# Performance work log

Measured on AMD Instinct MI355X. Metric: run time of the kernel, lower is better.

Reference implementation:

```python
import jax, jax.numpy as jnp
import numpy as np

B, L, DK, DV, H = 2, 2048, 512, 512, 8
DH_K = DK // H  # 64
DH_V = DV // H  # 64


def setup_inputs() -> dict:
    key = jax.random.key(0)
    ks = jax.random.split(key, 6)
    scale_w = 1.0 / np.sqrt(DK)
    return {
        "keys": jax.random.normal(ks[0], (B, L, DK), dtype=jnp.float32),
        "queries": jax.random.normal(ks[1], (B, L, DK), dtype=jnp.float32),
        "values": jax.random.normal(ks[2], (B, L, DV), dtype=jnp.float32),
        "WQ": jax.random.normal(ks[3], (H, DK, DH_K), dtype=jnp.float32) * scale_w,
        "WK": jax.random.normal(ks[4], (H, DK, DH_K), dtype=jnp.float32) * scale_w,
        "WV": jax.random.normal(ks[5], (H, DV, DH_V), dtype=jnp.float32) * scale_w,
    }


def reference(keys, queries, values, WQ, WK, WV):
    # Per-head projections, vectorized over all H heads at once.
    Q = jnp.einsum('bld,hde->bhle', queries, WQ)   # [B,H,Lq,dh]
    K = jnp.einsum('bld,hde->bhle', keys, WK)      # [B,H,Lk,dh]
    V = jnp.einsum('bld,hde->bhle', values, WV)    # [B,H,Lk,dv_h]
    Lk = keys.shape[1]
    # NOTE: original scales by sqrt(seq_len_k), not sqrt(head_dim).
    y = jnp.einsum('bhqe,bhke->bhqk', Q, K) / jnp.sqrt(jnp.float32(Lk))
    # NOTE: original applies softmax over torch dim=1 of [B,Lq,Lk],
    # i.e. the QUERY axis (axis=2 here in [B,H,Lq,Lk]).
    z = jax.nn.softmax(y, axis=2)
    out = jnp.einsum('bhqk,bhke->bhqe', z, V)      # [B,H,Lq,dv_h]
    # Concat heads on the feature dim (same order as torch.concat(..., 2)).
    Bq, Hh, Lq, Dh = out.shape
    return out.transpose(0, 2, 1, 3).reshape(Bq, Lq, Hh * Dh)
```

## Files before the change

### kernel.cpp

```cpp
#include <hip/hip_runtime.h>
#include <hip/hip_bf16.h>

#define LL 2048
#define DM 512
#define SCALE 0.02209708691207961f

typedef unsigned short u16;
typedef __attribute__((ext_vector_type(8))) short short8;
typedef __attribute__((ext_vector_type(4))) short short4v;
typedef __attribute__((ext_vector_type(4))) float f32x4;

#define XAQ_OFF 0u
#define XAK_OFF 2097152u
#define XAV_OFF 4194304u
#define WB_OFF  6291456u
#define QA_OFF  7077888u
#define KA_OFF  9175040u
#define VB_OFF  11272192u

__device__ __forceinline__ u16 f2bf(float f) {
  union { float f; unsigned u; } v; v.f = f;
  unsigned r = v.u + 0x7fff + ((v.u >> 16) & 1);
  return (u16)(r >> 16);
}
__device__ __forceinline__ float bf2f(u16 u) {
  union { unsigned u; float f; } v; v.u = ((unsigned)u) << 16; return v.f;
}
__device__ __forceinline__ size_t frag_idx(int bh, int t64, int w, int c, int lane) {
  return ((((size_t)(bh * 32 + t64) * 4 + w) * 2 + c) * 64 + lane) * 8;
}
__device__ __forceinline__ size_t vb_idx(int bh, int kt, int w, int et, int lane) {
  return ((((size_t)(bh * 32 + kt) * 4 + w) * 4 + et) * 64 + lane) * 4;
}

__global__ __launch_bounds__(256) void prep_kernel(
    const float* __restrict__ queries, const float* __restrict__ keys,
    const float* __restrict__ values, const float* __restrict__ WQ,
    const float* __restrict__ WK, const float* __restrict__ WV,
    u16* __restrict__ wsb) {
  int t = threadIdx.x;
  int blk = blockIdx.x;
  if (blk < 768) {
    int tens = blk >> 8;
    int grp  = blk & 255;
    const float* src = (tens == 0 ? queries : tens == 1 ? keys : values) +
                       (size_t)grp * 16 * 512;
    __shared__ __align__(16) u16 Xs[16][520];
#pragma unroll
    for (int rep = 0; rep < 8; ++rep) {
      int f4 = t + rep * 256;
      int row = f4 >> 7, c4 = f4 & 127;
      float4 v = *(const float4*)(src + (size_t)row * 512 + c4 * 4);
      short4v o;
      o[0] = (short)f2bf(v.x); o[1] = (short)f2bf(v.y);
      o[2] = (short)f2bf(v.z); o[3] = (short)f2bf(v.w);
      *(short4v*)&Xs[row][c4 * 4] = o;
    }
    __syncthreads();
    u16* dst = wsb + (tens == 0 ? XAQ_OFF : tens == 1 ? XAK_OFF : XAV_OFF) +
               (size_t)grp * 16 * 64 * 8;
#pragma unroll
    for (int rep = 0; rep < 4; ++rep) {
      int o = t + rep * 256;
      int kt = o >> 6, lane = o & 63;
      int quad = lane >> 4, l16 = lane & 15;
      short8 v = *(const short8*)&Xs[l16][kt * 32 + quad * 8];
      *(short8*)(dst + (size_t)o * 8) = v;
    }
  } else {
    int c2 = (blk - 768) * 256 + t;
    int lane = c2 & 63;
    int nt = (c2 >> 6) & 3;
    int kt = (c2 >> 8) & 15;
    int h  = (c2 >> 12) & 7;
    int z  = c2 >> 15;
    int quad = lane >> 4, l16 = lane & 15;
    const float* W = (z == 0) ? WQ : (z == 1) ? WK : WV;
    const float* src = W + ((size_t)h * DM + kt * 32 + quad * 8) * 64 + nt * 16 + l16;
    short8 o;
#pragma unroll
    for (int j = 0; j < 8; ++j) o[j] = (short)f2bf(src[(size_t)j * 64]);
    *(short8*)(wsb + WB_OFF + (size_t)c2 * 8) = o;
  }
}

__global__ __launch_bounds__(256) void proj_kernel(u16* __restrict__ wsb) {
  int t = threadIdx.x;
  int lane = t & 63, w = t >> 6, quad = lane >> 4, l16 = lane & 15;
  int z = blockIdx.z, bh = blockIdx.y, b = bh >> 3, h = bh & 7;
  int QT = blockIdx.x;

  const u16* Bw = wsb + WB_OFF + ((size_t)(z * 8 + h) * 16) * 4 * 64 * 8;
  const u16* Ab = wsb + (z == 0 ? XAQ_OFF : z == 1 ? XAK_OFF : XAV_OFF) +
      (((size_t)b * 128 + QT * 4 + w) * 16) * 64 * 8;

  f32x4 acc[4];
#pragma unroll
  for (int nt = 0; nt < 4; ++nt) acc[nt] = (f32x4){0.f, 0.f, 0.f, 0.f};

#pragma unroll 4
  for (int kt = 0; kt < 16; ++kt) {
    short8 a = *(const short8*)(Ab + ((size_t)kt * 64 + lane) * 8);
#pragma unroll
    for (int nt = 0; nt < 4; ++nt) {
      short8 bb = *(const short8*)(Bw + (((size_t)kt * 4 + nt) * 64 + lane) * 8);
      acc[nt] = __builtin_amdgcn_mfma_f32_16x16x32_bf16(a, bb, acc[nt], 0, 0, 0);
    }
  }

  __shared__ float Cs[64][68];
  float sc = (z == 0) ? SCALE : 1.0f;
#pragma unroll
  for (int nt = 0; nt < 4; ++nt)
#pragma unroll
    for (int r = 0; r < 4; ++r)
      Cs[w * 16 + quad * 4 + r][nt * 16 + l16] = acc[nt][r] * sc;
  __syncthreads();

  if (z < 2) {
    u16* base = wsb + (z == 0 ? QA_OFF : KA_OFF);
#pragma unroll
    for (int c = 0; c < 2; ++c) {
      const float* srcr = &Cs[w * 16 + l16][c * 32 + quad * 8];
      short8 o;
#pragma unroll
      for (int j = 0; j < 8; ++j) o[j] = (short)f2bf(srcr[j]);
      *(short8*)(base + frag_idx(bh, QT, w, c, lane)) = o;
    }
  } else {
#pragma unroll
    for (int et = 0; et < 4; ++et) {
      short4v o;
#pragma unroll
      for (int j = 0; j < 4; ++j)
        o[j] = (short)f2bf(Cs[w * 16 + quad * 4 + j][et * 16 + l16]);
      *(short4v*)(wsb + VB_OFF + vb_idx(bh, QT, w, et, lane)) = o;
    }
  }
}

__global__ __launch_bounds__(256) void stats_kernel(u16* __restrict__ wsb) {
  int t = threadIdx.x;
  int lane = t & 63, w = t >> 6, quad = lane >> 4, l16 = lane & 15;
  int bh = blockIdx.y;
  int KT = blockIdx.x;

  short8 ka[4][2];
#pragma unroll
  for (int mt = 0; mt < 4; ++mt)
#pragma unroll
    for (int c = 0; c < 2; ++c)
      ka[mt][c] = *(const short8*)(wsb + KA_OFF + frag_idx(bh, KT, mt, c, lane));

  float rs[4][4];
#pragma unroll
  for (int mt = 0; mt < 4; ++mt)
#pragma unroll
    for (int r = 0; r < 4; ++r) rs[mt][r] = 0.f;

  for (int qt = 0; qt < 32; ++qt) {
    short8 qb0 = *(const short8*)(wsb + QA_OFF + frag_idx(bh, qt, w, 0, lane));
    short8 qb1 = *(const short8*)(wsb + QA_OFF + frag_idx(bh, qt, w, 1, lane));
#pragma unroll
    for (int mt = 0; mt < 4; ++mt) {
      f32x4 y = (f32x4){0.f, 0.f, 0.f, 0.f};
      y = __builtin_amdgcn_mfma_f32_16x16x32_bf16(ka[mt][0], qb0, y, 0, 0, 0);
      y = __builtin_amdgcn_mfma_f32_16x16x32_bf16(ka[mt][1], qb1, y, 0, 0, 0);
#pragma unroll
      for (int r = 0; r < 4; ++r) rs[mt][r] += __expf(y[r]);
    }
  }
#pragma unroll
  for (int mt = 0; mt < 4; ++mt)
#pragma unroll
    for (int r = 0; r < 4; ++r) {
      rs[mt][r] += __shfl_xor(rs[mt][r], 1);
      rs[mt][r] += __shfl_xor(rs[mt][r], 2);
      rs[mt][r] += __shfl_xor(rs[mt][r], 4);
      rs[mt][r] += __shfl_xor(rs[mt][r], 8);
    }

  __shared__ float Sred[4][64];
  __shared__ float Ss[64];
  if (l16 == 0) {
#pragma unroll
    for (int mt = 0; mt < 4; ++mt)
#pragma unroll
      for (int r = 0; r < 4; ++r)
        Sred[w][mt * 16 + quad * 4 + r] = rs[mt][r];
  }
  __syncthreads();
  if (t < 64) Ss[t] = 1.0f / (Sred[0][t] + Sred[1][t] + Sred[2][t] + Sred[3][t]);
  __syncthreads();

#pragma unroll
  for (int et = 0; et < 4; ++et) {
    u16* p = wsb + VB_OFF + vb_idx(bh, KT, w, et, lane);
    short4v v = *(short4v*)p;
#pragma unroll
    for (int j = 0; j < 4; ++j)
      v[j] = (short)f2bf(bf2f((u16)v[j]) * Ss[w * 16 + quad * 4 + j]);
    *(short4v*)p = v;
  }
}

__global__ __launch_bounds__(256, 2) void attn_kernel(const u16* __restrict__ wsb,
                                                      float* __restrict__ out) {
  int t = threadIdx.x;
  int lane = t & 63, w = t >> 6, quad = lane >> 4, l16 = lane & 15;
  int bh = blockIdx.y, b = bh >> 3, h = bh & 7;
  int QT = blockIdx.x, qbase = QT * 64;

  short8 qf[4][2];
#pragma unroll
  for (int nt = 0; nt < 4; ++nt)
#pragma unroll
    for (int c = 0; c < 2; ++c)
      qf[nt][c] = *(const short8*)(wsb + QA_OFF + frag_idx(bh, QT, nt, c, lane));

  f32x4 oacc[4][4];
#pragma unroll
  for (int nt = 0; nt < 4; ++nt)
#pragma unroll
    for (int et = 0; et < 4; ++et) oacc[nt][et] = (f32x4){0.f, 0.f, 0.f, 0.f};

  for (int kt = 0; kt < 32; ++kt) {
    short8 ka0 = *(const short8*)(wsb + KA_OFF + frag_idx(bh, kt, w, 0, lane));
    short8 ka1 = *(const short8*)(wsb + KA_OFF + frag_idx(bh, kt, w, 1, lane));
    short4v vb[4];
#pragma unroll
    for (int et = 0; et < 4; ++et)
      vb[et] = *(const short4v*)(wsb + VB_OFF + vb_idx(bh, kt, w, et, lane));

#pragma unroll
    for (int nt = 0; nt < 4; ++nt) {
      f32x4 y = (f32x4){0.f, 0.f, 0.f, 0.f};
      y = __builtin_amdgcn_mfma_f32_16x16x32_bf16(ka0, qf[nt][0], y, 0, 0, 0);
      y = __builtin_amdgcn_mfma_f32_16x16x32_bf16(ka1, qf[nt][1], y, 0, 0, 0);
      short4v pa;
#pragma unroll
      for (int r = 0; r < 4; ++r) pa[r] = (short)f2bf(__expf(y[r]));
#pragma unroll
      for (int et = 0; et < 4; ++et)
        oacc[nt][et] = __builtin_amdgcn_mfma_f32_16x16x16bf16_1k(pa, vb[et], oacc[nt][et], 0, 0, 0);
    }
  }

  __shared__ float red[4][64][68];
#pragma unroll
  for (int nt = 0; nt < 4; ++nt)
#pragma unroll
    for (int et = 0; et < 4; ++et)
#pragma unroll
      for (int r = 0; r < 4; ++r)
        red[w][nt * 16 + quad * 4 + r][et * 16 + l16] = oacc[nt][et][r];
  __syncthreads();
  float* og = out + ((size_t)b * LL + qbase + w * 16) * 512 + h * 64;
#pragma unroll
  for (int i = 0; i < 16; ++i) {
    float s = red[0][w * 16 + i][lane] + red[1][w * 16 + i][lane] +
              red[2][w * 16 + i][lane] + red[3][w * 16 + i][lane];
    og[(size_t)i * 512 + lane] = s;
  }
}

extern "C" void kernel_launch(void* const* d_in, const int* in_sizes, int n_in,
                              void* d_out, int out_size, void* d_ws, size_t ws_size,
                              hipStream_t stream) {
  const float* keys    = (const float*)d_in[0];
  const float* queries = (const float*)d_in[1];
  const float* values  = (const float*)d_in[2];
  const float* WQ      = (const float*)d_in[3];
  const float* WK      = (const float*)d_in[4];
  const float* WV      = (const float*)d_in[5];
  float* out = (float*)d_out;
  u16* wsb = (u16*)d_ws;

  prep_kernel<<<dim3(768 + 384), 256, 0, stream>>>(queries, keys, values, WQ, WK, WV, wsb);
  proj_kernel<<<dim3(32, 16, 3), 256, 0, stream>>>(wsb);
  stats_kernel<<<dim3(32, 16), 256, 0, stream>>>(wsb);
  attn_kernel<<<dim3(32, 16), 256, 0, stream>>>(wsb, out);
}
```

Before: 143.4 us.

## Split stats and attention over key/query chunks with atomic sums and partial reduction

The stats kernel is split four ways along the query axis and accumulates column sums with atomicAdd into a zeroed float buffer. The attention kernel is split four ways along the key axis, applies the reciprocal normalisation inline instead of rescaling V, and writes partial outputs that a new reduce kernel sums. The goal is more blocks (2048 instead of 512) to fill the GPU's CUs. The cost is an extra launch, extra memory traffic for the partials, and atomic contention.

```diff
diff --git a/kernel.cpp b/kernel.cpp
--- a/kernel.cpp
+++ b/kernel.cpp
@@ -17,14 +17,13 @@
 #define QA_OFF  7077888u
 #define KA_OFF  9175040u
 #define VB_OFF  11272192u
+#define S_OFF   13369344u
+#define PART_OFF 13434880u
 
 __device__ __forceinline__ u16 f2bf(float f) {
   union { float f; unsigned u; } v; v.f = f;
   unsigned r = v.u + 0x7fff + ((v.u >> 16) & 1);
   return (u16)(r >> 16);
-}
-__device__ __forceinline__ float bf2f(u16 u) {
-  union { unsigned u; float f; } v; v.u = ((unsigned)u) << 16; return v.f;
 }
 __device__ __forceinline__ size_t frag_idx(int bh, int t64, int w, int c, int lane) {
   return ((((size_t)(bh * 32 + t64) * 4 + w) * 2 + c) * 64 + lane) * 8;
@@ -67,7 +66,7 @@
       short8 v = *(const short8*)&Xs[l16][kt * 32 + quad * 8];
       *(short8*)(dst + (size_t)o * 8) = v;
     }
-  } else {
+  } else if (blk < 1152) {
     int c2 = (blk - 768) * 256 + t;
     int lane = c2 & 63;
     int nt = (c2 >> 6) & 3;
@@ -81,6 +80,10 @@
 #pragma unroll
     for (int j = 0; j < 8; ++j) o[j] = (short)f2bf(src[(size_t)j * 64]);
     *(short8*)(wsb + WB_OFF + (size_t)c2 * 8) = o;
+  } else {
+    float* S = (float*)(wsb + S_OFF);
+    int idx = (blk - 1152) * 256 + t;
+    ((float4*)S)[idx] = (float4){0.f, 0.f, 0.f, 0.f};
   }
 }
 
@@ -139,11 +142,12 @@
   }
 }
 
-__global__ __launch_bounds__(256) void stats_kernel(u16* __restrict__ wsb) {
+__global__ __launch_bounds__(256, 4) void stats_kernel(u16* __restrict__ wsb) {
   int t = threadIdx.x;
   int lane = t & 63, w = t >> 6, quad = lane >> 4, l16 = lane & 15;
   int bh = blockIdx.y;
   int KT = blockIdx.x;
+  int qs = blockIdx.z;
 
   short8 ka[4][2];
 #pragma unroll
@@ -158,7 +162,7 @@
 #pragma unroll
     for (int r = 0; r < 4; ++r) rs[mt][r] = 0.f;
 
-  for (int qt = 0; qt < 32; ++qt) {
+  for (int qt = qs * 8; qt < qs * 8 + 8; ++qt) {
     short8 qb0 = *(const short8*)(wsb + QA_OFF + frag_idx(bh, qt, w, 0, lane));
     short8 qb1 = *(const short8*)(wsb + QA_OFF + frag_idx(bh, qt, w, 1, lane));
 #pragma unroll
@@ -181,7 +185,6 @@
     }
 
   __shared__ float Sred[4][64];
-  __shared__ float Ss[64];
   if (l16 == 0) {
 #pragma unroll
     for (int mt = 0; mt < 4; ++mt)
@@ -190,26 +193,21 @@
         Sred[w][mt * 16 + quad * 4 + r] = rs[mt][r];
   }
   __syncthreads();
-  if (t < 64) Ss[t] = 1.0f / (Sred[0][t] + Sred[1][t] + Sred[2][t] + Sred[3][t]);
-  __syncthreads();
-
-#pragma unroll
-  for (int et = 0; et < 4; ++et) {
-    u16* p = wsb + VB_OFF + vb_idx(bh, KT, w, et, lane);
-    short4v v = *(short4v*)p;
-#pragma unroll
-    for (int j = 0; j < 4; ++j)
-      v[j] = (short)f2bf(bf2f((u16)v[j]) * Ss[w * 16 + quad * 4 + j]);
-    *(short4v*)p = v;
-  }
-}
-
-__global__ __launch_bounds__(256, 2) void attn_kernel(const u16* __restrict__ wsb,
-                                                      float* __restrict__ out) {
+  if (t < 64) {
+    float s = Sred[0][t] + Sred[1][t] + Sred[2][t] + Sred[3][t];
+    float* S = (float*)(wsb + S_OFF);
+    atomicAdd(&S[(size_t)bh * LL + KT * 64 + t], s);
+  }
+}
+
+__global__ __launch_bounds__(256, 3) void attn_kernel(const u16* __restrict__ wsb,
+                                                      float* __restrict__ part) {
   int t = threadIdx.x;
   int lane = t & 63, w = t >> 6, quad = lane >> 4, l16 = lane & 15;
-  int bh = blockIdx.y, b = bh >> 3, h = bh & 7;
-  int QT = blockIdx.x, qbase = QT * 64;
+  int bh = blockIdx.y;
+  int QT = blockIdx.x;
+  int ks = blockIdx.z;
+  const float* S = (const float*)(wsb + S_OFF) + (size_t)bh * LL;
 
   short8 qf[4][2];
 #pragma unroll
@@ -224,13 +222,19 @@
 #pragma unroll
     for (int et = 0; et < 4; ++et) oacc[nt][et] = (f32x4){0.f, 0.f, 0.f, 0.f};
 
-  for (int kt = 0; kt < 32; ++kt) {
+  for (int kt = ks * 8; kt < ks * 8 + 8; ++kt) {
     short8 ka0 = *(const short8*)(wsb + KA_OFF + frag_idx(bh, kt, w, 0, lane));
     short8 ka1 = *(const short8*)(wsb + KA_OFF + frag_idx(bh, kt, w, 1, lane));
     short4v vb[4];
 #pragma unroll
     for (int et = 0; et < 4; ++et)
       vb[et] = *(const short4v*)(wsb + VB_OFF + vb_idx(bh, kt, w, et, lane));
+    float4 s4 = *(const float4*)(S + kt * 64 + w * 16 + quad * 4);
+    float si[4];
+    si[0] = __builtin_amdgcn_rcpf(s4.x);
+    si[1] = __builtin_amdgcn_rcpf(s4.y);
+    si[2] = __builtin_amdgcn_rcpf(s4.z);
+    si[3] = __builtin_amdgcn_rcpf(s4.w);
 
 #pragma unroll
     for (int nt = 0; nt < 4; ++nt) {
@@ -239,29 +243,63 @@
       y = __builtin_amdgcn_mfma_f32_16x16x32_bf16(ka1, qf[nt][1], y, 0, 0, 0);
       short4v pa;
 #pragma unroll
-      for (int r = 0; r < 4; ++r) pa[r] = (short)f2bf(__expf(y[r]));
+      for (int r = 0; r < 4; ++r) pa[r] = (short)f2bf(__expf(y[r]) * si[r]);
 #pragma unroll
       for (int et = 0; et < 4; ++et)
         oacc[nt][et] = __builtin_amdgcn_mfma_f32_16x16x16bf16_1k(pa, vb[et], oacc[nt][et], 0, 0, 0);
     }
   }
 
-  __shared__ float red[4][64][68];
-#pragma unroll
-  for (int nt = 0; nt < 4; ++nt)
-#pragma unroll
-    for (int et = 0; et < 4; ++et)
-#pragma unroll
-      for (int r = 0; r < 4; ++r)
-        red[w][nt * 16 + quad * 4 + r][et * 16 + l16] = oacc[nt][et][r];
+  __shared__ float red[2][64][68];
+  if (w >= 2) {
+#pragma unroll
+    for (int nt = 0; nt < 4; ++nt)
+#pragma unroll
+      for (int et = 0; et < 4; ++et)
+#pragma unroll
+        for (int r = 0; r < 4; ++r)
+          red[w - 2][nt * 16 + quad * 4 + r][et * 16 + l16] = oacc[nt][et][r];
+  }
   __syncthreads();
-  float* og = out + ((size_t)b * LL + qbase + w * 16) * 512 + h * 64;
+  if (w < 2) {
+#pragma unroll
+    for (int nt = 0; nt < 4; ++nt)
+#pragma unroll
+      for (int et = 0; et < 4; ++et)
+#pragma unroll
+        for (int r = 0; r < 4; ++r) {
+          float v = oacc[nt][et][r] + red[w][nt * 16 + quad * 4 + r][et * 16 + l16];
+          red[w][nt * 16 + quad * 4 + r][et * 16 + l16] = v;
+        }
+  }
+  __syncthreads();
+  float* pg = part + (((size_t)(ks * 16 + bh) * 32 + QT) * 64) * 64;
 #pragma unroll
   for (int i = 0; i < 16; ++i) {
-    float s = red[0][w * 16 + i][lane] + red[1][w * 16 + i][lane] +
-              red[2][w * 16 + i][lane] + red[3][w * 16 + i][lane];
-    og[(size_t)i * 512 + lane] = s;
-  }
+    float s = red[0][w * 16 + i][lane] + red[1][w * 16 + i][lane];
+    pg[(size_t)(w * 16 + i) * 64 + lane] = s;
+  }
+}
+
+__global__ __launch_bounds__(256) void reduce_kernel(const float* __restrict__ part,
+                                                     float* __restrict__ out) {
+  int g = blockIdx.x * 256 + threadIdx.x;
+  int e4 = g & 15;
+  int row = (g >> 4) & 63;
+  int QT = (g >> 10) & 31;
+  int bh = g >> 15;
+  size_t pidx = (((size_t)bh * 32 + QT) * 64 + row) * 64 + e4 * 4;
+  float4 a = *(const float4*)(part + pidx);
+  float4 b = *(const float4*)(part + pidx + 2097152);
+  float4 c = *(const float4*)(part + pidx + 2 * 2097152);
+  float4 d = *(const float4*)(part + pidx + 3 * 2097152);
+  float4 o;
+  o.x = a.x + b.x + c.x + d.x;
+  o.y = a.y + b.y + c.y + d.y;
+  o.z = a.z + b.z + c.z + d.z;
+  o.w = a.w + b.w + c.w + d.w;
+  int b_ = bh >> 3, h = bh & 7;
+  *(float4*)(out + ((size_t)(b_ * 2048 + QT * 64 + row) * 512) + h * 64 + e4 * 4) = o;
 }
 
 extern "C" void kernel_launch(void* const* d_in, const int* in_sizes, int n_in,
@@ -275,9 +313,11 @@
   const float* WV      = (const float*)d_in[5];
   float* out = (float*)d_out;
   u16* wsb = (u16*)d_ws;
-
-  prep_kernel<<<dim3(768 + 384), 256, 0, stream>>>(queries, keys, values, WQ, WK, WV, wsb);
+  float* part = (float*)(wsb + PART_OFF);
+
+  prep_kernel<<<dim3(1184), 256, 0, stream>>>(queries, keys, values, WQ, WK, WV, wsb);
   proj_kernel<<<dim3(32, 16, 3), 256, 0, stream>>>(wsb);
-  stats_kernel<<<dim3(32, 16), 256, 0, stream>>>(wsb);
-  attn_kernel<<<dim3(32, 16), 256, 0, stream>>>(wsb, out);
-}
+  stats_kernel<<<dim3(32, 16, 4), 256, 0, stream>>>(wsb);
+  attn_kernel<<<dim3(32, 16, 4), 256, 0, stream>>>(wsb, part);
+  reduce_kernel<<<dim3(2048), 256, 0, stream>>>(part, out);
+}
```

Result: slower. 196.9 us (+37.3%).
